# Kernel optimization log

Measured on AMD Instinct MI355X. Metric: run time of the kernel, lower is better.

The kernel has to match this reference:

```python
import jax, jax.numpy as jnp
import numpy as np

MAXGRAD = 2.0
B, H, W, C = 8, 512, 512, 16


def _integral_image(x):
    # x: [B,H,W,2]; cumsum x-channel along width, y-channel along height
    x_s = jnp.cumsum(x[..., 0], axis=2)
    y_s = jnp.cumsum(x[..., 1], axis=1)
    return jnp.stack([x_s, y_s], axis=-1) - 1.0


def _normalize(grid):
    # grid: [B,H,W,2] -> rescale each row/col extent to [0, W-1] x [0, H-1]
    Hh, Ww = grid.shape[1], grid.shape[2]
    max_x = grid[:, :, -1:, 0]  # [B,H,1]
    min_x = grid[:, :, :1, 0]
    max_y = grid[:, -1:, :, 1]  # [B,1,W]
    min_y = grid[:, :1, :, 1]
    norm_x = (grid[..., 0] - min_x) / (max_x - min_x)
    norm_y = (grid[..., 1] - min_y) / (max_y - min_y)
    return jnp.stack([(Ww - 1) * norm_x, (Hh - 1) * norm_y], axis=-1)


def _resample2d(im, grid):
    # im: [B,H,W,C], grid: [B,H,W,2] in pixel coords; bilinear with border clamp
    Bb, Hh, Ww, _ = im.shape
    x = grid[..., 0]
    y = grid[..., 1]
    x0 = jnp.floor(x).astype(jnp.int32)
    x1 = x0 + 1
    y0 = jnp.floor(y).astype(jnp.int32)
    y1 = y0 + 1
    x0 = jnp.clip(x0, 0, Ww - 1)
    x1 = jnp.clip(x1, 0, Ww - 1)
    y0 = jnp.clip(y0, 0, Hh - 1)
    y1 = jnp.clip(y1, 0, Hh - 1)
    b = jnp.arange(Bb)[:, None, None]
    Ia = im[b, y0, x0]  # [B,H,W,C]
    Ib = im[b, y1, x0]
    Ic = im[b, y0, x1]
    Id = im[b, y1, x1]
    x0f = x0.astype(x.dtype)
    x1f = x1.astype(x.dtype)
    y0f = y0.astype(y.dtype)
    y1f = y1.astype(y.dtype)
    wa = ((x1f - x) * (y1f - y))[..., None]
    wb = ((x1f - x) * (y - y0f))[..., None]
    wc = ((x - x0f) * (y1f - y))[..., None]
    wd = ((x - x0f) * (y - y0f))[..., None]
    return wa * Ia + wb * Ib + wc * Ic + wd * Id


def setup_inputs() -> dict:
    key = jax.random.key(0)
    k1, k2, k3 = jax.random.split(key, 3)
    mov = jax.random.normal(k1, (B, H, W, C), dtype=jnp.float32)
    ref = jax.random.normal(k2, (B, H, W, C), dtype=jnp.float32)
    defgrad = jax.random.normal(k3, (B, H, W, 2), dtype=jnp.float32) * 0.1
    return {"mov": mov, "ref": ref, "defgrad": defgrad}


def reference(mov, ref, defgrad):
    c = MAXGRAD
    dg = c / (1.0 + (c - 1.0) * jnp.exp(-defgrad))  # logistic growth
    base_grid = _integral_image(jnp.ones_like(dg))
    sampling_grid = _integral_image(dg)
    grid_norm = _normalize(sampling_grid)
    grid_inv = 2.0 * base_grid - grid_norm
    mov_def = _resample2d(mov, grid_norm)
    ref_def = _resample2d(mov_def, grid_inv)
    return (mov_def, ref_def, grid_norm, grid_inv)
```

## Files before the change

kernel.cpp:

```cpp
#include <hip/hip_runtime.h>

#define Bn 8
#define Hn 512
#define Wn 512
#define Cn 16

typedef float fx4 __attribute__((ext_vector_type(4)));

__device__ __forceinline__ float dgf(float g) { return 2.0f / (1.0f + __expf(-g)); }

__global__ __launch_bounds__(512) void grid_kernel(const float* __restrict__ defgrad,
                                                   float* __restrict__ grid_norm,
                                                   float* __restrict__ grid_inv) {
    const int wave = threadIdx.x >> 6;
    const int lane = threadIdx.x & 63;

    if (blockIdx.x < 64) {
        __shared__ float partial[8][64];
        const int b  = blockIdx.x >> 3;
        const int w0 = (blockIdx.x & 7) * 64;
        const int w  = w0 + lane;
        const long cbase = ((long)b * Hn) * Wn + w;

        float e0 = dgf(defgrad[cbase * 2 + 1]);
        float sum = 0.f;
        #pragma unroll 8
        for (int i = 0; i < 64; ++i) {
            int h = (wave << 6) + i;
            sum += dgf(defgrad[(cbase + (long)h * Wn) * 2 + 1]);
        }
        partial[wave][lane] = sum;
        __syncthreads();
        float off = 0.f, tot = 0.f;
        #pragma unroll
        for (int j = 0; j < 8; ++j) {
            float p = partial[j][lane];
            if (j < wave) off += p;
            tot += p;
        }
        float denom = tot - e0;
        float run = off;
        #pragma unroll 8
        for (int i = 0; i < 64; ++i) {
            int h = (wave << 6) + i;
            long pidx = cbase + (long)h * Wn;
            run += dgf(defgrad[pidx * 2 + 1]);
            float norm = (h == Hn - 1) ? 511.0f : 511.0f * ((run - e0) / denom);
            grid_norm[pidx * 2 + 1] = norm;
            grid_inv[pidx * 2 + 1]  = 2.0f * (float)h - norm;
        }
    } else {
        __shared__ float wsum[8];
        __shared__ float s0sh;
        const int row = blockIdx.x - 64;
        const int t   = threadIdx.x;
        const long base = (long)row * Wn;

        float v = dgf(defgrad[(base + t) * 2]);
        float x = v;
        #pragma unroll
        for (int o = 1; o < 64; o <<= 1) {
            float n = __shfl_up(x, o, 64);
            x += (lane >= o) ? n : 0.0f;
        }
        if (lane == 63) wsum[wave] = x;
        if (t == 0)     s0sh = v;
        __syncthreads();
        float pre = 0.f, tot = 0.f;
        #pragma unroll
        for (int j = 0; j < 8; ++j) {
            float p = wsum[j];
            if (j < wave) pre += p;
            tot += p;
        }
        float scan = x + pre;
        float s0   = s0sh;
        float norm = (t == Wn - 1) ? 511.0f : 511.0f * ((scan - s0) / (tot - s0));
        long o = (base + t) * 2;
        grid_norm[o] = norm;
        grid_inv[o]  = 2.0f * (float)t - norm;
    }
}

__global__ __launch_bounds__(256) void resample_kernel(const float* __restrict__ im,
                                                       const float* __restrict__ grid,
                                                       float* __restrict__ out) {
    const int tid = threadIdx.x;
    const int cg  = tid & 3;
    const int q   = tid >> 2;
    const long p0 = (long)blockIdx.x * 128 + q;
    const long p1 = p0 + 64;

    float2 g0 = *(const float2*)&grid[p0 * 2];
    float2 g1 = *(const float2*)&grid[p1 * 2];

    int x0a = (int)floorf(g0.x), y0a = (int)floorf(g0.y);
    int x1a = min(max(x0a + 1, 0), Wn - 1), y1a = min(max(y0a + 1, 0), Hn - 1);
    x0a = min(max(x0a, 0), Wn - 1);  y0a = min(max(y0a, 0), Hn - 1);
    int x0b = (int)floorf(g1.x), y0b = (int)floorf(g1.y);
    int x1b = min(max(x0b + 1, 0), Wn - 1), y1b = min(max(y0b + 1, 0), Hn - 1);
    x0b = min(max(x0b, 0), Wn - 1);  y0b = min(max(y0b, 0), Hn - 1);

    const float* base0 = im + ((p0 >> 18) << 22) + cg * 4;
    const float* base1 = im + ((p1 >> 18) << 22) + cg * 4;

    fx4 A0 = *(const fx4*)(base0 + (((long)(y0a << 9) + x0a) << 4));
    fx4 B0 = *(const fx4*)(base0 + (((long)(y1a << 9) + x0a) << 4));
    fx4 C0 = *(const fx4*)(base0 + (((long)(y0a << 9) + x1a) << 4));
    fx4 D0 = *(const fx4*)(base0 + (((long)(y1a << 9) + x1a) << 4));
    fx4 A1 = *(const fx4*)(base1 + (((long)(y0b << 9) + x0b) << 4));
    fx4 B1 = *(const fx4*)(base1 + (((long)(y1b << 9) + x0b) << 4));
    fx4 C1 = *(const fx4*)(base1 + (((long)(y0b << 9) + x1b) << 4));
    fx4 D1 = *(const fx4*)(base1 + (((long)(y1b << 9) + x1b) << 4));

    float wa0 = ((float)x1a - g0.x) * ((float)y1a - g0.y);
    float wb0 = ((float)x1a - g0.x) * (g0.y - (float)y0a);
    float wc0 = (g0.x - (float)x0a) * ((float)y1a - g0.y);
    float wd0 = (g0.x - (float)x0a) * (g0.y - (float)y0a);
    float wa1 = ((float)x1b - g1.x) * ((float)y1b - g1.y);
    float wb1 = ((float)x1b - g1.x) * (g1.y - (float)y0b);
    float wc1 = (g1.x - (float)x0b) * ((float)y1b - g1.y);
    float wd1 = (g1.x - (float)x0b) * (g1.y - (float)y0b);

    fx4 r0 = wa0 * A0 + wb0 * B0 + wc0 * C0 + wd0 * D0;
    fx4 r1 = wa1 * A1 + wb1 * B1 + wc1 * C1 + wd1 * D1;

    __builtin_nontemporal_store(r0, (fx4*)(out + (p0 << 4) + cg * 4));
    __builtin_nontemporal_store(r1, (fx4*)(out + (p1 << 4) + cg * 4));
}

extern "C" void kernel_launch(void* const* d_in, const int* in_sizes, int n_in,
                              void* d_out, int out_size, void* d_ws, size_t ws_size,
                              hipStream_t stream) {
    const float* mov     = (const float*)d_in[0];
    const float* defgrad = (const float*)d_in[2];
    float* out = (float*)d_out;

    const long N_img  = (long)Bn * Hn * Wn * Cn;
    const long N_grid = (long)Bn * Hn * Wn * 2;
    float* mov_def   = out;
    float* ref_def   = out + N_img;
    float* grid_norm = out + 2 * N_img;
    float* grid_inv  = out + 2 * N_img + N_grid;

    grid_kernel<<<dim3(64 + Bn * Hn), dim3(512), 0, stream>>>(defgrad, grid_norm, grid_inv);

    const int npix = Bn * Hn * Wn;
    resample_kernel<<<dim3(npix / 128), dim3(256), 0, stream>>>(mov, grid_norm, mov_def);
    resample_kernel<<<dim3(npix / 128), dim3(256), 0, stream>>>(mov_def, grid_inv, ref_def);
}
```

Baseline: 517.5 us.

## Fuse grid and two resample passes into one cooperative persistent kernel

Replaces the three launches (grid build plus two resamples) with one cooperative kernel of 1024 blocks that builds the grid, then runs both resample passes, separated by grid-wide syncs. Blocks are persistent: row scans loop over rows and each thread handles two columns, column scans use 128 blocks with 32 columns each, and each block resamples a contiguous 2048-pixel chunk remapped across blocks. This removes launch gaps and the tail of each kernel, but adds grid.sync costs, caps parallelism at 1024 resident blocks, and leaves the column-scan blocks as a serial bottleneck in the first phase.

```diff
diff --git a/kernel.cpp b/kernel.cpp
--- a/kernel.cpp
+++ b/kernel.cpp
@@ -1,98 +1,29 @@
 #include <hip/hip_runtime.h>
+#include <hip/hip_cooperative_groups.h>
+
+namespace cg = cooperative_groups;
 
 #define Bn 8
 #define Hn 512
 #define Wn 512
 #define Cn 16
+#define NBLK 1024
+#define NTHR 256
+#define NCOLB 128
 
 typedef float fx4 __attribute__((ext_vector_type(4)));
 
 __device__ __forceinline__ float dgf(float g) { return 2.0f / (1.0f + __expf(-g)); }
 
-__global__ __launch_bounds__(512) void grid_kernel(const float* __restrict__ defgrad,
-                                                   float* __restrict__ grid_norm,
-                                                   float* __restrict__ grid_inv) {
-    const int wave = threadIdx.x >> 6;
-    const int lane = threadIdx.x & 63;
-
-    if (blockIdx.x < 64) {
-        __shared__ float partial[8][64];
-        const int b  = blockIdx.x >> 3;
-        const int w0 = (blockIdx.x & 7) * 64;
-        const int w  = w0 + lane;
-        const long cbase = ((long)b * Hn) * Wn + w;
-
-        float e0 = dgf(defgrad[cbase * 2 + 1]);
-        float sum = 0.f;
-        #pragma unroll 8
-        for (int i = 0; i < 64; ++i) {
-            int h = (wave << 6) + i;
-            sum += dgf(defgrad[(cbase + (long)h * Wn) * 2 + 1]);
-        }
-        partial[wave][lane] = sum;
-        __syncthreads();
-        float off = 0.f, tot = 0.f;
-        #pragma unroll
-        for (int j = 0; j < 8; ++j) {
-            float p = partial[j][lane];
-            if (j < wave) off += p;
-            tot += p;
-        }
-        float denom = tot - e0;
-        float run = off;
-        #pragma unroll 8
-        for (int i = 0; i < 64; ++i) {
-            int h = (wave << 6) + i;
-            long pidx = cbase + (long)h * Wn;
-            run += dgf(defgrad[pidx * 2 + 1]);
-            float norm = (h == Hn - 1) ? 511.0f : 511.0f * ((run - e0) / denom);
-            grid_norm[pidx * 2 + 1] = norm;
-            grid_inv[pidx * 2 + 1]  = 2.0f * (float)h - norm;
-        }
-    } else {
-        __shared__ float wsum[8];
-        __shared__ float s0sh;
-        const int row = blockIdx.x - 64;
-        const int t   = threadIdx.x;
-        const long base = (long)row * Wn;
-
-        float v = dgf(defgrad[(base + t) * 2]);
-        float x = v;
-        #pragma unroll
-        for (int o = 1; o < 64; o <<= 1) {
-            float n = __shfl_up(x, o, 64);
-            x += (lane >= o) ? n : 0.0f;
-        }
-        if (lane == 63) wsum[wave] = x;
-        if (t == 0)     s0sh = v;
-        __syncthreads();
-        float pre = 0.f, tot = 0.f;
-        #pragma unroll
-        for (int j = 0; j < 8; ++j) {
-            float p = wsum[j];
-            if (j < wave) pre += p;
-            tot += p;
-        }
-        float scan = x + pre;
-        float s0   = s0sh;
-        float norm = (t == Wn - 1) ? 511.0f : 511.0f * ((scan - s0) / (tot - s0));
-        long o = (base + t) * 2;
-        grid_norm[o] = norm;
-        grid_inv[o]  = 2.0f * (float)t - norm;
-    }
-}
-
-__global__ __launch_bounds__(256) void resample_kernel(const float* __restrict__ im,
-                                                       const float* __restrict__ grid,
-                                                       float* __restrict__ out) {
-    const int tid = threadIdx.x;
-    const int cg  = tid & 3;
-    const int q   = tid >> 2;
-    const long p0 = (long)blockIdx.x * 128 + q;
+template<bool NT>
+__device__ __forceinline__ void resample_two(const float* __restrict__ im,
+                                             const float* __restrict__ grd,
+                                             float* __restrict__ outp,
+                                             long p0, int cg4)
+{
     const long p1 = p0 + 64;
-
-    float2 g0 = *(const float2*)&grid[p0 * 2];
-    float2 g1 = *(const float2*)&grid[p1 * 2];
+    float2 g0 = *(const float2*)&grd[p0 * 2];
+    float2 g1 = *(const float2*)&grd[p1 * 2];
 
     int x0a = (int)floorf(g0.x), y0a = (int)floorf(g0.y);
     int x1a = min(max(x0a + 1, 0), Wn - 1), y1a = min(max(y0a + 1, 0), Hn - 1);
@@ -101,8 +32,8 @@
     int x1b = min(max(x0b + 1, 0), Wn - 1), y1b = min(max(y0b + 1, 0), Hn - 1);
     x0b = min(max(x0b, 0), Wn - 1);  y0b = min(max(y0b, 0), Hn - 1);
 
-    const float* base0 = im + ((p0 >> 18) << 22) + cg * 4;
-    const float* base1 = im + ((p1 >> 18) << 22) + cg * 4;
+    const float* base0 = im + ((p0 >> 18) << 22) + cg4 * 4;
+    const float* base1 = im + ((p1 >> 18) << 22) + cg4 * 4;
 
     fx4 A0 = *(const fx4*)(base0 + (((long)(y0a << 9) + x0a) << 4));
     fx4 B0 = *(const fx4*)(base0 + (((long)(y1a << 9) + x0a) << 4));
@@ -125,8 +56,116 @@
     fx4 r0 = wa0 * A0 + wb0 * B0 + wc0 * C0 + wd0 * D0;
     fx4 r1 = wa1 * A1 + wb1 * B1 + wc1 * C1 + wd1 * D1;
 
-    __builtin_nontemporal_store(r0, (fx4*)(out + (p0 << 4) + cg * 4));
-    __builtin_nontemporal_store(r1, (fx4*)(out + (p1 << 4) + cg * 4));
+    if (NT) {
+        __builtin_nontemporal_store(r0, (fx4*)(outp + (p0 << 4) + cg4 * 4));
+        __builtin_nontemporal_store(r1, (fx4*)(outp + (p1 << 4) + cg4 * 4));
+    } else {
+        *(fx4*)(outp + (p0 << 4) + cg4 * 4) = r0;
+        *(fx4*)(outp + (p1 << 4) + cg4 * 4) = r1;
+    }
+}
+
+__global__ __launch_bounds__(NTHR, 4) void fused_kernel(
+    const float* __restrict__ mov,
+    const float* __restrict__ defgrad,
+    float* __restrict__ mov_def,
+    float* __restrict__ ref_def,
+    float* __restrict__ grid_norm,
+    float* __restrict__ grid_inv)
+{
+    cg::grid_group grid = cg::this_grid();
+    const int tid  = threadIdx.x;
+    const int wave = tid >> 6;
+    const int lane = tid & 63;
+    const int b    = blockIdx.x;
+
+    if (b < NCOLB) {
+        __shared__ float partial[8][32];
+        const int seg  = tid >> 5;
+        const int l32  = tid & 31;
+        const int bb   = b >> 4;
+        const int w    = ((b & 15) << 5) + l32;
+        const long cbase = ((long)bb * Hn) * Wn + w;
+
+        float e0 = dgf(defgrad[cbase * 2 + 1]);
+        float sum = 0.f;
+        #pragma unroll 8
+        for (int i = 0; i < 64; ++i) {
+            int h = (seg << 6) + i;
+            sum += dgf(defgrad[(cbase + (long)h * Wn) * 2 + 1]);
+        }
+        partial[seg][l32] = sum;
+        __syncthreads();
+        float off = 0.f, tot = 0.f;
+        #pragma unroll
+        for (int j = 0; j < 8; ++j) {
+            float p = partial[j][l32];
+            if (j < seg) off += p;
+            tot += p;
+        }
+        float denom = tot - e0;
+        float run = off;
+        #pragma unroll 4
+        for (int i = 0; i < 64; ++i) {
+            int h = (seg << 6) + i;
+            long pidx = cbase + (long)h * Wn;
+            run += dgf(defgrad[pidx * 2 + 1]);
+            float norm = (h == Hn - 1) ? 511.0f : 511.0f * ((run - e0) / denom);
+            grid_norm[pidx * 2 + 1] = norm;
+            grid_inv[pidx * 2 + 1]  = 2.0f * (float)h - norm;
+        }
+    } else {
+        __shared__ float wsum[4];
+        __shared__ float s0sh;
+        for (int row = b - NCOLB; row < Bn * Hn; row += NBLK - NCOLB) {
+            const long base = (long)row * Wn;
+            fx4 gq = *(const fx4*)&defgrad[(base + 2 * tid) * 2];
+            float v0 = dgf(gq.x), v1 = dgf(gq.z);
+            float s = v0 + v1;
+            float x = s;
+            #pragma unroll
+            for (int o = 1; o < 64; o <<= 1) {
+                float n = __shfl_up(x, o, 64);
+                x += (lane >= o) ? n : 0.0f;
+            }
+            if (lane == 63) wsum[wave] = x;
+            if (tid == 0)   s0sh = v0;
+            __syncthreads();
+            float pre = 0.f, tot = 0.f;
+            #pragma unroll
+            for (int j = 0; j < 4; ++j) {
+                float p = wsum[j];
+                if (j < wave) pre += p;
+                tot += p;
+            }
+            float excl  = pre + x - s;
+            float s0    = s0sh;
+            float denom = tot - s0;
+            float scan0 = excl + v0;
+            float scan1 = excl + v0 + v1;
+            int w0i = 2 * tid, w1i = 2 * tid + 1;
+            float n0 = 511.0f * ((scan0 - s0) / denom);
+            float n1 = (w1i == Wn - 1) ? 511.0f : 511.0f * ((scan1 - s0) / denom);
+            grid_norm[(base + w0i) * 2] = n0;
+            grid_inv [(base + w0i) * 2] = 2.0f * (float)w0i - n0;
+            grid_norm[(base + w1i) * 2] = n1;
+            grid_inv [(base + w1i) * 2] = 2.0f * (float)w1i - n1;
+            __syncthreads();
+        }
+    }
+
+    const int  lb  = ((b & 7) << 7) + (b >> 3);
+    const long pixbase = (long)lb * 2048;
+    const int  q   = tid >> 2;
+    const int  cg4 = tid & 3;
+
+    grid.sync();
+    for (int it = 0; it < 16; ++it)
+        resample_two<true>(mov, grid_norm, mov_def, pixbase + it * 128 + q, cg4);
+
+    grid.sync();
+    for (int it = 0; it < 16; ++it)
+        resample_two<true>(mov_def, grid_inv, ref_def, pixbase + it * 128 + q, cg4);
 }
 
 extern "C" void kernel_launch(void* const* d_in, const int* in_sizes, int n_in,
@@ -143,9 +182,8 @@
     float* grid_norm = out + 2 * N_img;
     float* grid_inv  = out + 2 * N_img + N_grid;
 
-    grid_kernel<<<dim3(64 + Bn * Hn), dim3(512), 0, stream>>>(defgrad, grid_norm, grid_inv);
-
-    const int npix = Bn * Hn * Wn;
-    resample_kernel<<<dim3(npix / 128), dim3(256), 0, stream>>>(mov, grid_norm, mov_def);
-    resample_kernel<<<dim3(npix / 128), dim3(256), 0, stream>>>(mov_def, grid_inv, ref_def);
+    void* args[] = { (void*)&mov, (void*)&defgrad, (void*)&mov_def,
+                     (void*)&ref_def, (void*)&grid_norm, (void*)&grid_inv };
+    hipLaunchCooperativeKernel((const void*)fused_kernel,
+                               dim3(NBLK), dim3(NTHR), args, 0, stream);
 }
```

After: 850.2 us. +64.3%, slower.
